# Kernel optimization log

Hardware: AMD Instinct MI355X
Metric: run time of the kernel (lower is better)

Reference implementation:

```python
import jax, jax.numpy as jnp
import numpy as np

B, T = 256, 4096
L = 128          # shapelet_length
K = 128          # num_shapelets
K_TOP = 5


def setup_inputs() -> dict:
    key = jax.random.key(0)
    kx, ks = jax.random.split(key)
    x = jax.random.normal(kx, (B, T), dtype=jnp.float32)
    shapelets = jax.random.normal(ks, (K, L), dtype=jnp.float32) * 0.1
    return {"x": x, "shapelets": shapelets}


def reference(x, shapelets):
    # x: [B, T], shapelets: [K, L]
    N = x.shape[1] - L + 1  # number of sliding windows
    # Gather overlapping windows: x_win [B, N, L]
    idx = jnp.arange(N)[:, None] + jnp.arange(L)[None, :]
    x_win = x[:, idx]
    # Per-window mean removal
    x_norm = x_win - jnp.mean(x_win, axis=2, keepdims=True)
    # Per-shapelet mean removal
    s_norm = shapelets - jnp.mean(shapelets, axis=1, keepdims=True)
    # Correlation: [B, N, K]
    corr = jnp.einsum('bnl,kl->bnk', x_norm, s_norm)
    k_val = min(K_TOP, N)
    # top-k over window dim N -> move N to last axis
    topk_vals, _ = jax.lax.top_k(jnp.transpose(corr, (0, 2, 1)), k_val)  # [B, K, k]
    p1 = topk_vals[:, :, 0]
    p2 = topk_vals[:, :, 1] if k_val >= 2 else p1
    p_mean = jnp.mean(topk_vals, axis=2)
    dominance = jax.nn.relu(p1 - p2)
    return jnp.concatenate([p1, p_mean, p2, dominance], axis=1)  # [B, 4K]
```

## Files before the change

kernel.cpp:

```cpp
#include <hip/hip_runtime.h>

#define T_LEN 4096
#define N_WIN 3969
#define K_SH  128
#define L_SH  128
#define B_SZ  256

#define SSTR  136
#define XSTR  4360

typedef __attribute__((ext_vector_type(8))) __bf16 bf16x8;
typedef __attribute__((ext_vector_type(4))) float f32x4;
typedef _Float16 h2 __attribute__((ext_vector_type(2)));

__device__ __forceinline__ unsigned short f2bf(float f) {
    union { float f; unsigned int u; } c; c.f = f;
    unsigned int u = c.u + 0x7fff + ((c.u >> 16) & 1u);
    return (unsigned short)(u >> 16);
}
__device__ __forceinline__ unsigned int pack2(unsigned short lo, unsigned short hi) {
    return (unsigned int)lo | ((unsigned int)hi << 16);
}

__device__ __forceinline__ h2 max2(h2 a, h2 b) { return __builtin_elementwise_max(a, b); }
__device__ __forceinline__ h2 min2(h2 a, h2 b) { return __builtin_elementwise_min(a, b); }
__device__ __forceinline__ h2 cvt2(float lo, float hi) {
    return __builtin_bit_cast(h2, __builtin_amdgcn_cvt_pkrtz(lo, hi));
}
__device__ __forceinline__ void ce2(h2& hi, h2& lo) {
    const h2 m = max2(hi, lo);
    lo = min2(hi, lo);
    hi = m;
}
__device__ __forceinline__ void sort4_2(h2& a, h2& b, h2& c, h2& d) {
    ce2(a, b); ce2(c, d); ce2(a, c); ce2(b, d); ce2(b, c);
}
__device__ __forceinline__ void merge44_top5_2(h2 a0, h2 a1, h2 a2, h2 a3,
                                               h2 b0, h2 b1, h2 b2, h2 b3,
                                               h2& r0, h2& r1, h2& r2, h2& r3, h2& r4) {
    ce2(a0, b0); ce2(a2, b2); ce2(b0, a2);
    ce2(a1, b1); ce2(a3, b3); ce2(b1, a3);
    r0 = a0;
    r1 = a1; r2 = b0; ce2(r1, r2);
    r3 = b1; r4 = a2; ce2(r3, r4);
}
__device__ __forceinline__ void merge55_2(h2& r0, h2& r1, h2& r2, h2& r3, h2& r4,
                                          h2 s0, h2 s1, h2 s2, h2 s3, h2 s4) {
    const h2 m00 = min2(r0, s0);
    const h2 m10 = min2(r1, s0), m01 = min2(r0, s1);
    const h2 m20 = min2(r2, s0), m11 = min2(r1, s1), m02 = min2(r0, s2);
    const h2 m30 = min2(r3, s0), m21 = min2(r2, s1), m12 = min2(r1, s2), m03 = min2(r0, s3);
    const h2 n0 = max2(r0, s0);
    const h2 n1 = max2(max2(r1, s1), m00);
    const h2 n2 = max2(max2(r2, s2), max2(m10, m01));
    const h2 n3 = max2(max2(max2(r3, s3), m20), max2(m11, m02));
    const h2 n4 = max2(max2(max2(r4, s4), max2(m30, m03)), max2(m21, m12));
    r0 = n0; r1 = n1; r2 = n2; r3 = n3; r4 = n4;
}
__device__ __forceinline__ void insert1_2(h2 v, h2* rt) {
    h2 b = max2(rt[4], v); h2 m;
    m = max2(rt[3], b);     b     = min2(rt[3], b);     rt[3] = m;
    m = max2(rt[2], rt[3]); rt[3] = min2(rt[2], rt[3]); rt[2] = m;
    m = max2(rt[1], rt[2]); rt[2] = min2(rt[1], rt[2]); rt[1] = m;
    m = max2(rt[0], rt[1]); rt[1] = min2(rt[0], rt[1]); rt[0] = m;
    rt[4] = b;
}
__device__ __forceinline__ void select32(const f32x4* acc0, const f32x4* acc1, h2* rt) {
    h2 p[16];
    #pragma unroll
    for (int m = 0; m < 4; ++m)
        #pragma unroll
        for (int i = 0; i < 4; ++i)
            p[4 * m + i] = cvt2(acc0[m][i], acc1[m][i]);
    sort4_2(p[0], p[1], p[2],  p[3]);
    sort4_2(p[4], p[5], p[6],  p[7]);
    sort4_2(p[8], p[9], p[10], p[11]);
    sort4_2(p[12], p[13], p[14], p[15]);
    h2 u0, u1, u2, u3, u4, v0, v1, v2, v3, v4;
    merge44_top5_2(p[0], p[1], p[2],  p[3],  p[4],  p[5],  p[6],  p[7],  u0, u1, u2, u3, u4);
    merge44_top5_2(p[8], p[9], p[10], p[11], p[12], p[13], p[14], p[15], v0, v1, v2, v3, v4);
    merge55_2(u0, u1, u2, u3, u4, v0, v1, v2, v3, v4);
    merge55_2(rt[0], rt[1], rt[2], rt[3], rt[4], u0, u1, u2, u3, u4);
}

__global__ __launch_bounds__(512, 2)
void shapelet_fused8_kernel(const float* __restrict__ x,
                            const float* __restrict__ s,
                            float* __restrict__ out) {
    __shared__ __align__(16) unsigned short ldsS[K_SH * SSTR];
    __shared__ __align__(16) unsigned short ldsX[8 * XSTR];

    const int t    = threadIdx.x;
    const int lane = t & 63;
    const int w    = t >> 6;
    const int r    = lane & 15;
    const int q    = lane >> 4;
    const int c7   = lane & 7;
    const int ub   = (lane >> 3) & 1;
    const int g    = w >> 2;
    const int mh   = (w >> 1) & 1;
    const int wp   = w & 1;
    const int mtb  = 4 * mh;
    const int b    = blockIdx.x;

    {
        const int k = t >> 2, e4 = t & 3;
        const float4* srow = (const float4*)(s + k * L_SH + e4 * 32);
        float4 v[8];
        float sum = 0.0f;
        #pragma unroll
        for (int j = 0; j < 8; ++j) {
            v[j] = srow[j];
            sum += (v[j].x + v[j].y) + (v[j].z + v[j].w);
        }
        sum += __shfl_xor(sum, 1);
        sum += __shfl_xor(sum, 2);
        const float mean = sum * (1.0f / 128.0f);
        uint4* dst = (uint4*)((char*)ldsS + k * (SSTR * 2) + e4 * 64);
        #pragma unroll
        for (int j = 0; j < 4; ++j) {
            uint4 o;
            o.x = pack2(f2bf(v[2*j].x - mean),   f2bf(v[2*j].y - mean));
            o.y = pack2(f2bf(v[2*j].z - mean),   f2bf(v[2*j].w - mean));
            o.z = pack2(f2bf(v[2*j+1].x - mean), f2bf(v[2*j+1].y - mean));
            o.w = pack2(f2bf(v[2*j+1].z - mean), f2bf(v[2*j+1].w - mean));
            dst[j] = o;
        }
        if (e4 == 3) *(uint4*)((char*)ldsS + k * (SSTR * 2) + 256) = make_uint4(0,0,0,0);
    }

    {
        const float* __restrict__ xb = x + (size_t)b * T_LEN;
        const int a = (t ^ (t >> 3)) & 7;
        for (int i = (t >> 3); i < XSTR / 8; i += 64) {
            const int p0 = 8 * i;
            float xv[16];
            if (p0 + 16 <= T_LEN) {
                const float4* sp = (const float4*)(xb + p0);
                #pragma unroll
                for (int j = 0; j < 4; ++j) *(float4*)(xv + 4 * j) = sp[j];
            } else {
                #pragma unroll
                for (int j = 0; j < 16; ++j) {
                    const int gi = p0 + j;
                    xv[j] = (gi < T_LEN) ? xb[gi] : 0.0f;
                }
            }
            unsigned short bv[16];
            #pragma unroll
            for (int j = 0; j < 16; ++j) bv[j] = f2bf(xv[j]);
            uint4 o;
            o.x = pack2(bv[a],     bv[a + 1]);
            o.y = pack2(bv[a + 2], bv[a + 3]);
            o.z = pack2(bv[a + 4], bv[a + 5]);
            o.w = pack2(bv[a + 6], bv[a + 7]);
            *(uint4*)((char*)ldsX + a * (XSTR * 2) + 2 * p0) = o;
        }
    }
    __syncthreads();

    bf16x8 bfr[4][4];
    #pragma unroll
    for (int kt = 0; kt < 4; ++kt)
        #pragma unroll
        for (int c = 0; c < 4; ++c)
            bfr[kt][c] = __builtin_bit_cast(bf16x8, *(const uint4*)(
                (const char*)ldsS + ((64 * wp + 16 * kt + r)) * (SSTR * 2) + 64 * c + 16 * q));

    h2 rtP[5], rtQ[5];
    #pragma unroll
    for (int i = 0; i < 5; ++i) {
        rtP[i] = __builtin_bit_cast(h2, 0xFC00FC00u);
        rtQ[i] = __builtin_bit_cast(h2, 0xFC00FC00u);
    }

    const char* xp = (const char*)ldsX + c7 * (XSTR * 2) + 16 * q + 16 * ub + 32 * mtb
                   + g * 256;

    const f32x4 ZCC = (f32x4){0.f, 0.f, 0.f, 0.f};

#define TILE_STEP                                                               \
    {                                                                           \
        bf16x8 afr[10];                                                         \
        _Pragma("unroll")                                                       \
        for (int j = 0; j < 10; ++j)                                            \
            afr[j] = __builtin_bit_cast(bf16x8, *(const uint4*)(xp + 32 * j));  \
        xp += 512;                                                              \
        f32x4 acc0[4], acc1[4];                                                 \
        _Pragma("unroll")                                                       \
        for (int m = 0; m < 4; ++m) {                                           \
            acc0[m] = __builtin_amdgcn_mfma_f32_16x16x32_bf16(afr[m], bfr[0][0], ZCC, 0, 0, 0); \
            acc1[m] = __builtin_amdgcn_mfma_f32_16x16x32_bf16(afr[m], bfr[1][0], ZCC, 0, 0, 0); \
        }                                                                       \
        _Pragma("unroll")                                                       \
        for (int c = 1; c < 4; ++c) {                                           \
            _Pragma("unroll")                                                   \
            for (int m = 0; m < 4; ++m) {                                       \
                acc0[m] = __builtin_amdgcn_mfma_f32_16x16x32_bf16(afr[m + 2*c], bfr[0][c], acc0[m], 0, 0, 0); \
                acc1[m] = __builtin_amdgcn_mfma_f32_16x16x32_bf16(afr[m + 2*c], bfr[1][c], acc1[m], 0, 0, 0); \
            }                                                                   \
        }                                                                       \
        select32(acc0, acc1, rtP);                                              \
        _Pragma("unroll")                                                       \
        for (int m = 0; m < 4; ++m) {                                           \
            acc0[m] = __builtin_amdgcn_mfma_f32_16x16x32_bf16(afr[m], bfr[2][0], ZCC, 0, 0, 0); \
            acc1[m] = __builtin_amdgcn_mfma_f32_16x16x32_bf16(afr[m], bfr[3][0], ZCC, 0, 0, 0); \
        }                                                                       \
        _Pragma("unroll")                                                       \
        for (int c = 1; c < 4; ++c) {                                           \
            _Pragma("unroll")                                                   \
            for (int m = 0; m < 4; ++m) {                                       \
                acc0[m] = __builtin_amdgcn_mfma_f32_16x16x32_bf16(afr[m + 2*c], bfr[2][c], acc0[m], 0, 0, 0); \
                acc1[m] = __builtin_amdgcn_mfma_f32_16x16x32_bf16(afr[m + 2*c], bfr[3][c], acc1[m], 0, 0, 0); \
            }                                                                   \
        }                                                                       \
        select32(acc0, acc1, rtQ);                                              \
    }

    const int nst = (g == 0) ? 16 : 15;
    for (int st = 0; st < nst; ++st) { TILE_STEP }
#undef TILE_STEP

    if (g == 1 && mh == 0) {
        f32x4 e[4];
        #pragma unroll
        for (int kt = 0; kt < 4; ++kt) e[kt] = (f32x4){0.f, 0.f, 0.f, 0.f};
        const char* eb = (const char*)ldsX + c7 * (XSTR * 2) + 7936 + 16 * q + 16 * ub;
        #pragma unroll
        for (int c = 0; c < 4; ++c) {
            const bf16x8 af = __builtin_bit_cast(bf16x8, *(const uint4*)(eb + 64 * c));
            #pragma unroll
            for (int kt = 0; kt < 4; ++kt)
                e[kt] = __builtin_amdgcn_mfma_f32_16x16x32_bf16(af, bfr[kt][c], e[kt], 0, 0, 0);
        }
        if (q == 0) {
            insert1_2(cvt2(e[0][0], e[1][0]), rtP);
            insert1_2(cvt2(e[2][0], e[3][0]), rtQ);
        }
    }

    #pragma unroll
    for (int mask = 16; mask <= 32; mask <<= 1) {
        h2 sv[5], sw[5];
        #pragma unroll
        for (int i = 0; i < 5; ++i) {
            sv[i] = __builtin_bit_cast(h2, __shfl_xor(__builtin_bit_cast(int, rtP[i]), mask));
            sw[i] = __builtin_bit_cast(h2, __shfl_xor(__builtin_bit_cast(int, rtQ[i]), mask));
        }
        merge55_2(rtP[0], rtP[1], rtP[2], rtP[3], rtP[4], sv[0], sv[1], sv[2], sv[3], sv[4]);
        merge55_2(rtQ[0], rtQ[1], rtQ[2], rtQ[3], rtQ[4], sw[0], sw[1], sw[2], sw[3], sw[4]);
    }

    __syncthreads();
    unsigned int* pbuf = (unsigned int*)ldsS;
    const int gm = g * 2 + mh;
    if (gm != 0 && q == 0) {
        unsigned int* p = pbuf + ((wp * 3 + (gm - 1)) * 16 + r) * 10;
        #pragma unroll
        for (int i = 0; i < 5; ++i) {
            p[i]     = __builtin_bit_cast(unsigned int, rtP[i]);
            p[5 + i] = __builtin_bit_cast(unsigned int, rtQ[i]);
        }
    }
    __syncthreads();
    if (gm == 0 && q == 0) {
        #pragma unroll
        for (int reg = 0; reg < 3; ++reg) {
            const unsigned int* p = pbuf + ((wp * 3 + reg) * 16 + r) * 10;
            h2 sv[5], sw[5];
            #pragma unroll
            for (int i = 0; i < 5; ++i) {
                sv[i] = __builtin_bit_cast(h2, p[i]);
                sw[i] = __builtin_bit_cast(h2, p[5 + i]);
            }
            merge55_2(rtP[0], rtP[1], rtP[2], rtP[3], rtP[4], sv[0], sv[1], sv[2], sv[3], sv[4]);
            merge55_2(rtQ[0], rtQ[1], rtQ[2], rtQ[3], rtQ[4], sw[0], sw[1], sw[2], sw[3], sw[4]);
        }

        float* ob = out + (size_t)b * (4 * K_SH);
        const h2* rts[2] = { rtP, rtQ };
        #pragma unroll
        for (int setI = 0; setI < 2; ++setI) {
            const h2* rt = rts[setI];
            const float A0 = (float)rt[0][0], A1 = (float)rt[1][0], A2 = (float)rt[2][0],
                        A3 = (float)rt[3][0], A4 = (float)rt[4][0];
            const float B0 = (float)rt[0][1], B1 = (float)rt[1][1], B2 = (float)rt[2][1],
                        B3 = (float)rt[3][1], B4 = (float)rt[4][1];
            const int ksA = 64 * wp + 32 * setI + r, ksB = ksA + 16;
            const float mA = (((A0 + A1) + (A2 + A3)) + A4) * 0.2f;
            const float mB = (((B0 + B1) + (B2 + B3)) + B4) * 0.2f;
            ob[ksA]           = A0;
            ob[K_SH + ksA]    = mA;
            ob[2*K_SH + ksA]  = A1;
            ob[3*K_SH + ksA]  = fmaxf(A0 - A1, 0.0f);
            ob[ksB]           = B0;
            ob[K_SH + ksB]    = mB;
            ob[2*K_SH + ksB]  = B1;
            ob[3*K_SH + ksB]  = fmaxf(B0 - B1, 0.0f);
        }
    }
}

extern "C" void kernel_launch(void* const* d_in, const int* in_sizes, int n_in,
                              void* d_out, int out_size, void* d_ws, size_t ws_size,
                              hipStream_t stream) {
    const float* x = (const float*)d_in[0];
    const float* s = (const float*)d_in[1];
    float* out = (float*)d_out;
    shapelet_fused8_kernel<<<B_SZ, 512, 0, stream>>>(x, s, out);
}
```

Measured before the change: 98.23 us.

## Double block to 16 waves, splitting window tiles across eight wave groups

Launches 1024 threads per batch element and distributes the sliding-window tiles round-robin over eight wave-pair groups instead of four. Shapelet and input staging loops are re-split for the larger block, and the final cross-wave top-5 merge now combines seven partial results per wave pair. The aim is more waves per CU to hide MFMA and LDS latency, at the cost of a longer reduction tail and tighter register limits from the stricter launch bounds.

```diff
diff --git a/kernel.cpp b/kernel.cpp
--- a/kernel.cpp
+++ b/kernel.cpp
@@ -83,10 +83,10 @@
     merge55_2(rt[0], rt[1], rt[2], rt[3], rt[4], u0, u1, u2, u3, u4);
 }
 
-__global__ __launch_bounds__(512, 2)
-void shapelet_fused8_kernel(const float* __restrict__ x,
-                            const float* __restrict__ s,
-                            float* __restrict__ out) {
+__global__ __launch_bounds__(1024, 4)
+void shapelet_fused16_kernel(const float* __restrict__ x,
+                             const float* __restrict__ s,
+                             float* __restrict__ out) {
     __shared__ __align__(16) unsigned short ldsS[K_SH * SSTR];
     __shared__ __align__(16) unsigned short ldsX[8 * XSTR];
 
@@ -97,28 +97,27 @@
     const int q    = lane >> 4;
     const int c7   = lane & 7;
     const int ub   = (lane >> 3) & 1;
-    const int g    = w >> 2;
-    const int mh   = (w >> 1) & 1;
     const int wp   = w & 1;
-    const int mtb  = 4 * mh;
+    const int G    = w >> 1;
     const int b    = blockIdx.x;
 
     {
-        const int k = t >> 2, e4 = t & 3;
-        const float4* srow = (const float4*)(s + k * L_SH + e4 * 32);
-        float4 v[8];
+        const int k = t >> 3, e8 = t & 7;
+        const float4* srow = (const float4*)(s + k * L_SH + e8 * 16);
+        float4 v[4];
         float sum = 0.0f;
         #pragma unroll
-        for (int j = 0; j < 8; ++j) {
+        for (int j = 0; j < 4; ++j) {
             v[j] = srow[j];
             sum += (v[j].x + v[j].y) + (v[j].z + v[j].w);
         }
         sum += __shfl_xor(sum, 1);
         sum += __shfl_xor(sum, 2);
+        sum += __shfl_xor(sum, 4);
         const float mean = sum * (1.0f / 128.0f);
-        uint4* dst = (uint4*)((char*)ldsS + k * (SSTR * 2) + e4 * 64);
-        #pragma unroll
-        for (int j = 0; j < 4; ++j) {
+        uint4* dst = (uint4*)((char*)ldsS + k * (SSTR * 2) + e8 * 32);
+        #pragma unroll
+        for (int j = 0; j < 2; ++j) {
             uint4 o;
             o.x = pack2(f2bf(v[2*j].x - mean),   f2bf(v[2*j].y - mean));
             o.y = pack2(f2bf(v[2*j].z - mean),   f2bf(v[2*j].w - mean));
@@ -126,13 +125,13 @@
             o.w = pack2(f2bf(v[2*j+1].z - mean), f2bf(v[2*j+1].w - mean));
             dst[j] = o;
         }
-        if (e4 == 3) *(uint4*)((char*)ldsS + k * (SSTR * 2) + 256) = make_uint4(0,0,0,0);
+        if (e8 == 7) *(uint4*)((char*)ldsS + k * (SSTR * 2) + 256) = make_uint4(0,0,0,0);
     }
 
     {
         const float* __restrict__ xb = x + (size_t)b * T_LEN;
         const int a = (t ^ (t >> 3)) & 7;
-        for (int i = (t >> 3); i < XSTR / 8; i += 64) {
+        for (int i = (t >> 3); i < XSTR / 8; i += 128) {
             const int p0 = 8 * i;
             float xv[16];
             if (p0 + 16 <= T_LEN) {
@@ -174,8 +173,8 @@
         rtQ[i] = __builtin_bit_cast(h2, 0xFC00FC00u);
     }
 
-    const char* xp = (const char*)ldsX + c7 * (XSTR * 2) + 16 * q + 16 * ub + 32 * mtb
-                   + g * 256;
+    const char* xp = (const char*)ldsX + c7 * (XSTR * 2) + 16 * q + 16 * ub
+                   + G * 128;
 
     const f32x4 ZCC = (f32x4){0.f, 0.f, 0.f, 0.f};
 
@@ -185,7 +184,7 @@
         _Pragma("unroll")                                                       \
         for (int j = 0; j < 10; ++j)                                            \
             afr[j] = __builtin_bit_cast(bf16x8, *(const uint4*)(xp + 32 * j));  \
-        xp += 512;                                                              \
+        xp += 1024;                                                             \
         f32x4 acc0[4], acc1[4];                                                 \
         _Pragma("unroll")                                                       \
         for (int m = 0; m < 4; ++m) {                                           \
@@ -217,11 +216,11 @@
         select32(acc0, acc1, rtQ);                                              \
     }
 
-    const int nst = (g == 0) ? 16 : 15;
+    const int nst = (G < 6) ? 8 : 7;
     for (int st = 0; st < nst; ++st) { TILE_STEP }
 #undef TILE_STEP
 
-    if (g == 1 && mh == 0) {
+    if (G == 6) {
         f32x4 e[4];
         #pragma unroll
         for (int kt = 0; kt < 4; ++kt) e[kt] = (f32x4){0.f, 0.f, 0.f, 0.f};
@@ -253,9 +252,8 @@
 
     __syncthreads();
     unsigned int* pbuf = (unsigned int*)ldsS;
-    const int gm = g * 2 + mh;
-    if (gm != 0 && q == 0) {
-        unsigned int* p = pbuf + ((wp * 3 + (gm - 1)) * 16 + r) * 10;
+    if (G != 0 && q == 0) {
+        unsigned int* p = pbuf + ((wp * 7 + (G - 1)) * 16 + r) * 10;
         #pragma unroll
         for (int i = 0; i < 5; ++i) {
             p[i]     = __builtin_bit_cast(unsigned int, rtP[i]);
@@ -263,10 +261,10 @@
         }
     }
     __syncthreads();
-    if (gm == 0 && q == 0) {
-        #pragma unroll
-        for (int reg = 0; reg < 3; ++reg) {
-            const unsigned int* p = pbuf + ((wp * 3 + reg) * 16 + r) * 10;
+    if (G == 0 && q == 0) {
+        #pragma unroll
+        for (int reg = 0; reg < 7; ++reg) {
+            const unsigned int* p = pbuf + ((wp * 7 + reg) * 16 + r) * 10;
             h2 sv[5], sw[5];
             #pragma unroll
             for (int i = 0; i < 5; ++i) {
@@ -307,5 +305,5 @@
     const float* x = (const float*)d_in[0];
     const float* s = (const float*)d_in[1];
     float* out = (float*)d_out;
-    shapelet_fused8_kernel<<<B_SZ, 512, 0, stream>>>(x, s, out);
-}
+    shapelet_fused16_kernel<<<B_SZ, 1024, 0, stream>>>(x, s, out);
+}
```

New measurement: 128.3 us. +30.6%, slower.
